# Performance work log

Measured on AMD Instinct MI355X. Metric: run time of the kernel, lower is better.

Reference implementation:

```python
import jax, jax.numpy as jnp
import numpy as np

B, L, DIM = 8, 512, 8          # batch, seq len, raw channels (value dim D = 2*DIM = 16)
ET, HID, H = 128, 128, 2       # embed_time, hidden_size, num_heads
MAXLEN = 512
NEG = -1e9


def setup_inputs() -> dict:
    key = jax.random.key(0)
    ks = jax.random.split(key, 40)
    def n(i, shape, s=0.05):
        return jax.random.normal(ks[i], shape, jnp.float32) * s
    vals = jax.random.normal(ks[0], (B, L, DIM), jnp.float32)
    msk = (jax.random.uniform(ks[1], (B, L, DIM)) > 0.2).astype(jnp.float32)
    x = jnp.concatenate([vals, msk], -1)                      # (B, L, 2*DIM)
    time_steps = jax.random.uniform(ks[2], (B, L), jnp.float32)
    return {
        'x': x, 'time_steps': time_steps,
        # learned time embedding: Linear(1, ET-1) periodic + Linear(1,1)
        'w_per': n(3, (1, ET - 1)), 'b_per': n(4, (ET - 1,)),
        'w_lin': n(5, (1, 1)), 'b_lin': n(6, (1,)),
        # MultiTimeAttention projections
        'Wq_t': n(7, (ET, ET)), 'bq_t': n(8, (ET,)),
        'Wk_t': n(9, (ET, ET)), 'bk_t': n(10, (ET,)),
        'Wo_t': n(11, (2 * DIM * H, HID)), 'bo_t': n(12, (HID,)),
        'pos_emb': n(13, (MAXLEN + 1, HID)), 'cls_emb': n(14, (1, HID)),
        # transformer block (BERT-style post-LN encoder layer, d_ff=HID)
        'tWq': n(15, (HID, HID)), 'tbq': n(16, (HID,)),
        'tWk': n(17, (HID, HID)), 'tbk': n(18, (HID,)),
        'tWv': n(19, (HID, HID)), 'tbv': n(20, (HID,)),
        'tWo': n(21, (HID, HID)), 'tbo': n(22, (HID,)),
        'ln1_g': jnp.ones((HID,), jnp.float32), 'ln1_b': jnp.zeros((HID,), jnp.float32),
        'fW1': n(23, (HID, HID)), 'fb1': n(24, (HID,)),
        'fW2': n(25, (HID, HID)), 'fb2': n(26, (HID,)),
        'ln2_g': jnp.ones((HID,), jnp.float32), 'ln2_b': jnp.zeros((HID,), jnp.float32),
        # BertPooler
        'pW': n(27, (HID, HID)), 'pb': n(28, (HID,)),
    }


def _time_emb(tt, w_per, b_per, w_lin, b_lin):
    tt = tt[..., None]                                        # (B, L, 1)
    return jnp.concatenate([tt @ w_lin + b_lin, jnp.sin(tt @ w_per + b_per)], -1)


def _ln(x, g, b, eps=1e-5):
    m = x.mean(-1, keepdims=True)
    v = ((x - m) ** 2).mean(-1, keepdims=True)
    return (x - m) / jnp.sqrt(v + eps) * g + b


def _mta(q_emb, k_emb, value, mask, Wq, bq, Wk, bk, Wo, bo):
    # MultiTimeAttention: scores broadcast to value-channel axis, softmax over keys
    D = value.shape[-1]
    dk = ET // H
    def split(e, W, b):
        p = e @ W + b
        return p.reshape(e.shape[0], -1, H, dk).transpose(0, 2, 1, 3)
    q = split(q_emb, Wq, bq)                                  # (Bq, H, Lq, dk)
    k = split(k_emb, Wk, bk)                                  # (B,  H, Lk, dk)
    scores = jnp.matmul(q, k.swapaxes(-1, -2)) / jnp.sqrt(jnp.float32(dk))  # (B,H,Lq,Lk)
    s5 = jnp.where(mask[:, None, None, :, :] == 0, NEG, scores[..., None])  # (B,H,Lq,Lk,D)
    p = jax.nn.softmax(s5, axis=-2)
    out = jnp.einsum('bhqkd,bkd->bhqd', p, value)             # (B, H, Lq, D)
    Bv = value.shape[0]
    out = out.transpose(0, 2, 1, 3).reshape(Bv, -1, H * D)
    return out @ Wo + bo


def _tblock(x, tWq, tbq, tWk, tbk, tWv, tbv, tWo, tbo, ln1_g, ln1_b,
            fW1, fb1, fW2, fb2, ln2_g, ln2_b):
    Bq, Lq, _ = x.shape
    dk = HID // H
    def heads(W, b):
        return (x @ W + b).reshape(Bq, Lq, H, dk).transpose(0, 2, 1, 3)
    q, k, v = heads(tWq, tbq), heads(tWk, tbk), heads(tWv, tbv)
    a = jax.nn.softmax(jnp.matmul(q, k.swapaxes(-1, -2)) / jnp.sqrt(jnp.float32(dk)), -1)
    o = jnp.matmul(a, v).transpose(0, 2, 1, 3).reshape(Bq, Lq, HID) @ tWo + tbo
    x = _ln(x + o, ln1_g, ln1_b)
    f = jax.nn.relu(x @ fW1 + fb1) @ fW2 + fb2
    return _ln(x + f, ln2_g, ln2_b)


def reference(x, time_steps, w_per, b_per, w_lin, b_lin,
              Wq_t, bq_t, Wk_t, bk_t, Wo_t, bo_t, pos_emb, cls_emb,
              tWq, tbq, tWk, tbk, tWv, tbv, tWo, tbo, ln1_g, ln1_b,
              fW1, fb1, fW2, fb2, ln2_g, ln2_b, pW, pb):
    Bx = x.shape[0]
    mask_half = x[:, :, DIM:]
    mask = jnp.concatenate([mask_half, mask_half], -1)        # (B, L, 2*DIM)
    key_e = _time_emb(time_steps, w_per, b_per, w_lin, b_lin)
    tq_e = _time_emb(time_steps, w_per, b_per, w_lin, b_lin)  # query_time_steps=None -> same
    cls_t = jnp.linspace(0.0, 1.0, 128, dtype=jnp.float32)[None]
    cls_q_e = _time_emb(cls_t, w_per, b_per, w_lin, b_lin)    # (1, 128, ET)
    cls_out = _mta(cls_q_e, key_e, x, mask, Wq_t, bq_t, Wk_t, bk_t, Wo_t, bo_t)
    out = _mta(tq_e, key_e, x, mask, Wq_t, bq_t, Wk_t, bk_t, Wo_t, bo_t)
    tb = (tWq, tbq, tWk, tbk, tWv, tbv, tWo, tbo, ln1_g, ln1_b,
          fW1, fb1, fW2, fb2, ln2_g, ln2_b)
    cls_repr = jnp.broadcast_to(cls_emb[None, :, :], (Bx, 1, HID))
    # encode(cls_out, is_pooling=True), pooling='bert': no pos emb, take token 0
    h = _tblock(jnp.concatenate([cls_repr, cls_out], 1), *tb)
    cls_pooling = jnp.tanh(h[:, 0] @ pW + pb)                 # (B, HID)
    # encode(out, is_pooling=False) [pretrain path]: pos emb + transformer, drop CLS
    h2 = jnp.concatenate([cls_repr, out], 1)                  # (B, L+1, HID)
    h2 = h2 + pos_emb[:h2.shape[1]][None]
    h2 = _tblock(h2, *tb)
    last_hidden_state = h2[:, 1:]                             # (B, L, HID)
    return cls_pooling, last_hidden_state
```

## Files before the change

### kernel.cpp

```cpp
#include <hip/hip_runtime.h>
#include <hip/hip_bf16.h>
#include <math.h>


static constexpr int NM_ = 8 * 513;
static constexpr int NC_ = 8 * 129;
static constexpr int NT_ = NM_ + NC_;

using bf = __hip_bfloat16;
typedef __attribute__((ext_vector_type(8))) short bf16x8;
typedef __attribute__((ext_vector_type(4))) short bf16x4;
typedef __attribute__((ext_vector_type(4))) float floatx4;
typedef __attribute__((ext_vector_type(8))) unsigned short ushortx8;

__device__ __forceinline__ float wave_reduce_sum(float v) {
    #pragma unroll
    for (int off = 32; off >= 1; off >>= 1) v += __shfl_xor(v, off);
    return v;
}
__device__ __forceinline__ float wave_reduce_max(float v) {
    #pragma unroll
    for (int off = 32; off >= 1; off >>= 1) v = fmaxf(v, __shfl_xor(v, off));
    return v;
}
__device__ __forceinline__ float u2f(unsigned short u) {
    return __uint_as_float(((unsigned)u) << 16);
}
__device__ __forceinline__ unsigned short f2u(float f) {
    unsigned u = __float_as_uint(f);
    return (unsigned short)((u + 0x7FFF + ((u >> 16) & 1)) >> 16);
}
__device__ __forceinline__ bf16x8 join8(bf16x4 lo, bf16x4 hi) {
    return __builtin_shufflevector(lo, hi, 0, 1, 2, 3, 4, 5, 6, 7);
}
__device__ __forceinline__ float rdin(const void* p, int i, int flag) {
    return flag ? u2f(((const unsigned short*)p)[i]) : ((const float*)p)[i];
}

struct PrepAll {
    const void* src[32]; int n[32]; int dstoff[32]; int conv[32];
    const void* wsrc[8]; unsigned short* wdst[8]; float wscale[8];
    const void* ts; const void* w_per; const void* b_per;
    const void* w_lin; const void* b_lin;
    unsigned short* key_e16;
    const unsigned short* det;
};
__global__ void prep_all_kernel(PrepAll a, float* dst) {
    int flag = (a.det[0] == 0x3F80u) ? 1 : 0;
    int blk = blockIdx.x, tid = threadIdx.x;
    if (blk < 8224) {
        int which = blk / 257, bi = blk - which * 257;
        if (!a.conv[which]) return;
        int i = bi * 256 + tid;
        if (i < a.n[which]) dst[a.dstoff[which] + i] = rdin(a.src[which], i, flag);
    } else if (blk < 8736) {
        int p = blk - 8224;
        int m = p >> 6;
        int idx = (p & 63) * 256 + tid;
        int c = idx >> 9;
        int l = (idx >> 3) & 63;
        int j = idx & 7;
        int k = (c >> 3) * 32 + (l >> 4) * 8 + j;
        int n = (c & 7) * 16 + (l & 15);
        a.wdst[m][idx] = f2u(rdin(a.wsrc[m], k * 128 + n, flag) * a.wscale[m]);
    } else {
        int p = blk - 8736;
        int row = p * 2 + (tid >> 7), j = tid & 127;
        float t = (row < 4096) ? rdin(a.ts, row, flag)
                               : (float)(row - 4096) * (1.0f / 127.0f);
        float v;
        if (j == 0) v = t * rdin(a.w_lin, 0, flag) + rdin(a.b_lin, 0, flag);
        else        v = sinf(t * rdin(a.w_per, j - 1, flag) + rdin(a.b_per, j - 1, flag));
        a.key_e16[row * 128 + j] = f2u(v);
    }
}

struct GemmM {
    const void* A[3]; const unsigned short* W[3]; const float* bias[3];
    unsigned short* C[3];
    int M[3]; int act[3]; int abf[3]; float bscale[3];
};
__global__ void __launch_bounds__(256)
gemm_mfma_kernel(GemmM p) {
    int y = blockIdx.y;
    const unsigned short* Wsw = p.W[y];
    const float* bias = p.bias[y];
    unsigned short* C = p.C[y];
    int M = p.M[y], act = p.act[y], abf = p.abf[y];
    float bscale = p.bscale[y];
    int m0 = blockIdx.x * 16;
    if (m0 >= M) return;
    __shared__ unsigned short As[16][136];
    int tid = threadIdx.x;
    if (abf) {
        const unsigned short* A = (const unsigned short*)p.A[y];
        int r = tid >> 4, c0 = (tid & 15) * 8;
        ushortx8 v = {0, 0, 0, 0, 0, 0, 0, 0};
        if (m0 + r < M) v = *(const ushortx8*)(A + (size_t)(m0 + r) * 128 + c0);
        *(ushortx8*)&As[r][c0] = v;
    } else {
        const float* A = (const float*)p.A[y];
        int r = tid >> 4, c0 = (tid & 15) * 8;
        float4 v0 = make_float4(0.f, 0.f, 0.f, 0.f), v1 = v0;
        if (m0 + r < M) {
            v0 = *(const float4*)(A + (size_t)(m0 + r) * 128 + c0);
            v1 = *(const float4*)(A + (size_t)(m0 + r) * 128 + c0 + 4);
        }
        *(ushort4*)&As[r][c0] = make_ushort4(f2u(v0.x), f2u(v0.y), f2u(v0.z), f2u(v0.w));
        *(ushort4*)&As[r][c0 + 4] = make_ushort4(f2u(v1.x), f2u(v1.y), f2u(v1.z), f2u(v1.w));
    }
    __syncthreads();

    int wv = tid >> 6, lane = tid & 63;
    floatx4 acc0 = {0.f, 0.f, 0.f, 0.f}, acc1 = acc0;
    int am = lane & 15, aq = lane >> 4;
    #pragma unroll
    for (int ks = 0; ks < 4; ++ks) {
        bf16x8 af = *(bf16x8*)&As[am][ks * 32 + aq * 8];
        const unsigned short* base = Wsw + ((size_t)ks * 8 + 2 * wv) * 512 + lane * 8;
        bf16x8 b0 = *(const bf16x8*)(base);
        bf16x8 b1 = *(const bf16x8*)(base + 512);
        acc0 = __builtin_amdgcn_mfma_f32_16x16x32_bf16(af, b0, acc0, 0, 0, 0);
        acc1 = __builtin_amdgcn_mfma_f32_16x16x32_bf16(af, b1, acc1, 0, 0, 0);
    }
    int col = lane & 15, rowb = (lane >> 4) * 4;
    #pragma unroll
    for (int t = 0; t < 2; ++t) {
        floatx4 acc = t ? acc1 : acc0;
        int n = wv * 32 + t * 16 + col;
        float bv = bias[n] * bscale;
        #pragma unroll
        for (int rg = 0; rg < 4; ++rg) {
            int m = m0 + rowb + rg;
            if (m < M) {
                float o = acc[rg] + bv;
                if (act) o = fmaxf(o, 0.f);
                C[(size_t)m * 128 + n] = f2u(o);
            }
        }
    }
}

__global__ void __launch_bounds__(256)
gemm_mfma_ln_kernel(const unsigned short* A, const unsigned short* Wsw, const float* bias,
                    const float* resid, const float* gam, const float* bet,
                    float* C) {
    int m0 = blockIdx.x * 16;
    __shared__ unsigned short As[16][136];
    __shared__ float redS[4][4][4], redQ[4][4][4];
    __shared__ float smean[16], sinv[16];
    int tid = threadIdx.x;
    {
        int r = tid >> 4, c0 = (tid & 15) * 8;
        ushortx8 v = *(const ushortx8*)(A + (size_t)(m0 + r) * 128 + c0);
        *(ushortx8*)&As[r][c0] = v;
    }
    __syncthreads();

    int wv = tid >> 6, lane = tid & 63;
    floatx4 acc0 = {0.f, 0.f, 0.f, 0.f}, acc1 = acc0;
    int am = lane & 15, aq = lane >> 4;
    #pragma unroll
    for (int ks = 0; ks < 4; ++ks) {
        bf16x8 af = *(bf16x8*)&As[am][ks * 32 + aq * 8];
        const unsigned short* base = Wsw + ((size_t)ks * 8 + 2 * wv) * 512 + lane * 8;
        bf16x8 b0 = *(const bf16x8*)(base);
        bf16x8 b1 = *(const bf16x8*)(base + 512);
        acc0 = __builtin_amdgcn_mfma_f32_16x16x32_bf16(af, b0, acc0, 0, 0, 0);
        acc1 = __builtin_amdgcn_mfma_f32_16x16x32_bf16(af, b1, acc1, 0, 0, 0);
    }

    int col = lane & 15, g = lane >> 4, rowb = g * 4;
    float ov[2][4];
    #pragma unroll
    for (int t = 0; t < 2; ++t) {
        int n = wv * 32 + t * 16 + col;
        float bv = bias[n];
        floatx4 acc = t ? acc1 : acc0;
        #pragma unroll
        for (int rg = 0; rg < 4; ++rg)
            ov[t][rg] = acc[rg] + bv + resid[(size_t)(m0 + rowb + rg) * 128 + n];
    }
    #pragma unroll
    for (int rg = 0; rg < 4; ++rg) {
        float s = ov[0][rg] + ov[1][rg];
        float q = ov[0][rg] * ov[0][rg] + ov[1][rg] * ov[1][rg];
        #pragma unroll
        for (int off = 8; off >= 1; off >>= 1) {
            s += __shfl_xor(s, off);
            q += __shfl_xor(q, off);
        }
        if ((lane & 15) == 0) { redS[wv][g][rg] = s; redQ[wv][g][rg] = q; }
    }
    __syncthreads();
    if (tid < 16) {
        int gg = tid >> 2, rg = tid & 3;
        float s = redS[0][gg][rg] + redS[1][gg][rg] + redS[2][gg][rg] + redS[3][gg][rg];
        float q = redQ[0][gg][rg] + redQ[1][gg][rg] + redQ[2][gg][rg] + redQ[3][gg][rg];
        float mean = s * 0.0078125f;
        float var = q * 0.0078125f - mean * mean;
        smean[tid] = mean;
        sinv[tid] = rsqrtf(var + 1e-5f);
    }
    __syncthreads();
    #pragma unroll
    for (int t = 0; t < 2; ++t) {
        int n = wv * 32 + t * 16 + col;
        float gm = gam[n], bb = bet[n];
        #pragma unroll
        for (int rg = 0; rg < 4; ++rg) {
            int row = rowb + rg;
            C[(size_t)(m0 + row) * 128 + n] = (ov[t][rg] - smean[row]) * sinv[row] * gm + bb;
        }
    }
}

__global__ void __launch_bounds__(256)
ffn_ln_kernel(const float* x1, const unsigned short* W1, const float* b1,
              const unsigned short* W2, const float* b2,
              const float* gam, const float* bet, float* dout, float* x2c) {
    int m0 = blockIdx.x * 16;
    __shared__ float Xs[16][128];
    __shared__ unsigned short As[16][136];
    __shared__ unsigned short Hs[16][136];
    __shared__ float redS[4][4][4], redQ[4][4][4];
    __shared__ float smean[16], sinv[16];
    int tid = threadIdx.x;
    {
        int r = tid >> 4, c0 = (tid & 15) * 8;
        float4 v0 = *(const float4*)(x1 + (size_t)(m0 + r) * 128 + c0);
        float4 v1 = *(const float4*)(x1 + (size_t)(m0 + r) * 128 + c0 + 4);
        *(float4*)&Xs[r][c0] = v0;
        *(float4*)&Xs[r][c0 + 4] = v1;
        *(ushort4*)&As[r][c0] = make_ushort4(f2u(v0.x), f2u(v0.y), f2u(v0.z), f2u(v0.w));
        *(ushort4*)&As[r][c0 + 4] = make_ushort4(f2u(v1.x), f2u(v1.y), f2u(v1.z), f2u(v1.w));
    }
    __syncthreads();

    int wv = tid >> 6, lane = tid & 63;
    int am = lane & 15, aq = lane >> 4;
    int col = lane & 15, g = lane >> 4, rowb = g * 4;

    {
        floatx4 acc0 = {0.f, 0.f, 0.f, 0.f}, acc1 = acc0;
        #pragma unroll
        for (int ks = 0; ks < 4; ++ks) {
            bf16x8 af = *(bf16x8*)&As[am][ks * 32 + aq * 8];
            const unsigned short* base = W1 + ((size_t)ks * 8 + 2 * wv) * 512 + lane * 8;
            bf16x8 bb0 = *(const bf16x8*)(base);
            bf16x8 bb1 = *(const bf16x8*)(base + 512);
            acc0 = __builtin_amdgcn_mfma_f32_16x16x32_bf16(af, bb0, acc0, 0, 0, 0);
            acc1 = __builtin_amdgcn_mfma_f32_16x16x32_bf16(af, bb1, acc1, 0, 0, 0);
        }
        #pragma unroll
        for (int t = 0; t < 2; ++t) {
            int n = wv * 32 + t * 16 + col;
            float bv = b1[n];
            floatx4 acc = t ? acc1 : acc0;
            #pragma unroll
            for (int rg = 0; rg < 4; ++rg)
                Hs[rowb + rg][n] = f2u(fmaxf(acc[rg] + bv, 0.f));
        }
    }
    __syncthreads();

    floatx4 acc0 = {0.f, 0.f, 0.f, 0.f}, acc1 = acc0;
    #pragma unroll
    for (int ks = 0; ks < 4; ++ks) {
        bf16x8 af = *(bf16x8*)&Hs[am][ks * 32 + aq * 8];
        const unsigned short* base = W2 + ((size_t)ks * 8 + 2 * wv) * 512 + lane * 8;
        bf16x8 bb0 = *(const bf16x8*)(base);
        bf16x8 bb1 = *(const bf16x8*)(base + 512);
        acc0 = __builtin_amdgcn_mfma_f32_16x16x32_bf16(af, bb0, acc0, 0, 0, 0);
        acc1 = __builtin_amdgcn_mfma_f32_16x16x32_bf16(af, bb1, acc1, 0, 0, 0);
    }
    float ov[2][4];
    #pragma unroll
    for (int t = 0; t < 2; ++t) {
        int n = wv * 32 + t * 16 + col;
        float bv = b2[n];
        floatx4 acc = t ? acc1 : acc0;
        #pragma unroll
        for (int rg = 0; rg < 4; ++rg)
            ov[t][rg] = acc[rg] + bv + Xs[rowb + rg][n];
    }
    #pragma unroll
    for (int rg = 0; rg < 4; ++rg) {
        float s = ov[0][rg] + ov[1][rg];
        float q = ov[0][rg] * ov[0][rg] + ov[1][rg] * ov[1][rg];
        #pragma unroll
        for (int off = 8; off >= 1; off >>= 1) {
            s += __shfl_xor(s, off);
            q += __shfl_xor(q, off);
        }
        if ((lane & 15) == 0) { redS[wv][g][rg] = s; redQ[wv][g][rg] = q; }
    }
    __syncthreads();
    if (tid < 16) {
        int gg = tid >> 2, rg = tid & 3;
        float s = redS[0][gg][rg] + redS[1][gg][rg] + redS[2][gg][rg] + redS[3][gg][rg];
        float q = redQ[0][gg][rg] + redQ[1][gg][rg] + redQ[2][gg][rg] + redQ[3][gg][rg];
        float mean = s * 0.0078125f;
        float var = q * 0.0078125f - mean * mean;
        smean[tid] = mean;
        sinv[tid] = rsqrtf(var + 1e-5f);
    }
    __syncthreads();
    #pragma unroll
    for (int t = 0; t < 2; ++t) {
        int n = wv * 32 + t * 16 + col;
        float gm = gam[n], bb = bet[n];
        #pragma unroll
        for (int rg = 0; rg < 4; ++rg) {
            int row = rowb + rg;
            int m = m0 + row;
            float val = (ov[t][rg] - smean[row]) * sinv[row] * gm + bb;
            if (m < NM_) {
                int b = m / 513, r = m - b * 513;
                if (r >= 1)
                    dout[1024 + (size_t)b * 65536 + (size_t)(r - 1) * 128 + n] = val;
            } else {
                int mc = m - NM_;
                int b = mc / 129, r = mc - b * 129;
                if (r == 0) x2c[b * 128 + n] = val;
            }
        }
    }
}

__global__ void mta_out_assemble_kernel(const float* att, const float* W, const float* bias,
                                        const float* cls_emb, const float* pos, float* xin) {
    int tid = threadIdx.x;
    if (blockIdx.x == 320) {
        for (int e = tid; e < 16 * 128; e += 256) {
            int i = e >> 7, j = e & 127;
            int b = i >> 1;
            if ((i & 1) == 0) xin[(size_t)(b * 513) * 128 + j] = cls_emb[j] + pos[j];
            else              xin[(size_t)(4104 + b * 129) * 128 + j] = cls_emb[j];
        }
        return;
    }
    int m0 = blockIdx.x * 16;
    __shared__ float As[16][36];
    int r = tid >> 4, gq = tid & 15, c0 = gq * 8;
    if (gq < 2) {
        const float* src = att + (size_t)(m0 + r) * 32 + gq * 16;
        *(float4*)&As[r][gq * 16]      = *(const float4*)(src);
        *(float4*)&As[r][gq * 16 + 4]  = *(const float4*)(src + 4);
        *(float4*)&As[r][gq * 16 + 8]  = *(const float4*)(src + 8);
        *(float4*)&As[r][gq * 16 + 12] = *(const float4*)(src + 12);
    }
    __syncthreads();
    float acc[8];
    #pragma unroll
    for (int j = 0; j < 8; ++j) acc[j] = bias[c0 + j];
    #pragma unroll 8
    for (int k = 0; k < 32; ++k) {
        float a = As[r][k];
        const float4 w0 = *(const float4*)(W + (size_t)k * 128 + c0);
        const float4 w1 = *(const float4*)(W + (size_t)k * 128 + c0 + 4);
        acc[0] = fmaf(a, w0.x, acc[0]); acc[1] = fmaf(a, w0.y, acc[1]);
        acc[2] = fmaf(a, w0.z, acc[2]); acc[3] = fmaf(a, w0.w, acc[3]);
        acc[4] = fmaf(a, w1.x, acc[4]); acc[5] = fmaf(a, w1.y, acc[5]);
        acc[6] = fmaf(a, w1.z, acc[6]); acc[7] = fmaf(a, w1.w, acc[7]);
    }
    int m = m0 + r;
    size_t dstrow;
    if (m < 1024) {
        int b = m >> 7, rr = m & 127;
        dstrow = (size_t)(4104 + b * 129 + 1 + rr);
    } else {
        int mm = m - 1024;
        int b = mm >> 9, rr = mm & 511;
        dstrow = (size_t)(b * 513 + 1 + rr);
        const float* pr = pos + (size_t)(1 + rr) * 128 + c0;
        float4 p0 = *(const float4*)(pr);
        float4 p1 = *(const float4*)(pr + 4);
        acc[0] += p0.x; acc[1] += p0.y; acc[2] += p0.z; acc[3] += p0.w;
        acc[4] += p1.x; acc[5] += p1.y; acc[6] += p1.z; acc[7] += p1.w;
    }
    *(float4*)(xin + dstrow * 128 + c0) = make_float4(acc[0], acc[1], acc[2], acc[3]);
    *(float4*)(xin + dstrow * 128 + c0 + 4) = make_float4(acc[4], acc[5], acc[6], acc[7]);
}

__global__ void __launch_bounds__(256)
mta_att_kernel(const unsigned short* qp_cls, const unsigned short* qp_main,
               const unsigned short* kp, const float* x,
               float* att_cls, float* att_mn) {
    int is_cls = (blockIdx.x >= 32);
    int qt = is_cls ? (blockIdx.x - 32) : blockIdx.x;
    int h = blockIdx.y, b = blockIdx.z;
    int tid = threadIdx.x, lane = tid & 63, wv = tid >> 6;
    __shared__ unsigned short Qs[16][72];
    __shared__ unsigned short KV[64][72];
    __shared__ unsigned short sp[16][520];
    __shared__ unsigned short Bt[16][520];
    float* xv = (float*)&KV[0][0];
    int q0 = qt * 16;

    if (tid < 128) {
        int r = tid >> 3, c0 = (tid & 7) * 8;
        const unsigned short* qrow = is_cls ? (qp_cls + (size_t)(q0 + r) * 128 + h * 64)
                                            : (qp_main + (size_t)(b * 512 + q0 + r) * 128 + h * 64);
        *(ushortx8*)&Qs[r][c0] = *(const ushortx8*)(qrow + c0);
    }
    __syncthreads();

    bf16x8 qf0, qf1;
    {
        int m = lane & 15, g = lane >> 4;
        qf0 = *(const bf16x8*)&Qs[m][g * 8];
        qf1 = *(const bf16x8*)&Qs[m][32 + g * 8];
    }

    for (int kt = 0; kt < 8; ++kt) {
        int k0 = kt * 64;
        {
            int kk = tid >> 3, e0 = (tid & 7) * 8;
            #pragma unroll
            for (int it = 0; it < 2; ++it, kk += 32)
                *(ushortx8*)&KV[kk][e0] =
                    *(const ushortx8*)(kp + (size_t)(b * 512 + k0 + kk) * 128 + h * 64 + e0);
        }
        __syncthreads();
        int kn = lane & 15, g = lane >> 4;
        floatx4 acc = {0.f, 0.f, 0.f, 0.f};
        {
            bf16x8 b0 = *(const bf16x8*)&KV[wv * 16 + kn][g * 8];
            acc = __builtin_amdgcn_mfma_f32_16x16x32_bf16(qf0, b0, acc, 0, 0, 0);
            bf16x8 b1 = *(const bf16x8*)&KV[wv * 16 + kn][32 + g * 8];
            acc = __builtin_amdgcn_mfma_f32_16x16x32_bf16(qf1, b1, acc, 0, 0, 0);
        }
        int colk = k0 + wv * 16 + kn;
        #pragma unroll
        for (int rg = 0; rg < 4; ++rg) sp[g * 4 + rg][colk] = f2u(acc[rg]);
        __syncthreads();
    }

    for (int rr = wv; rr < 16; rr += 4) {
        float m = -1e30f;
        for (int k = lane; k < 512; k += 64) m = fmaxf(m, u2f(sp[rr][k]));
        m = wave_reduce_max(m);
        for (int k = lane; k < 512; k += 64) sp[rr][k] = f2u(expf(u2f(sp[rr][k]) - m));
    }

    for (int kt = 0; kt < 8; ++kt) {
        int k0 = kt * 64;
        __syncthreads();
        {
            int kk = tid >> 2, c0 = (tid & 3) * 4;
            float4 v = *(const float4*)(x + (size_t)(b * 512 + k0 + kk) * 16 + c0);
            xv[kk * 17 + c0] = v.x; xv[kk * 17 + c0 + 1] = v.y;
            xv[kk * 17 + c0 + 2] = v.z; xv[kk * 17 + c0 + 3] = v.w;
        }
        __syncthreads();
        {
            int c = tid & 15, k4 = (tid >> 4) * 4;
            #pragma unroll
            for (int i = 0; i < 4; ++i) {
                int k = k4 + i;
                float val = (c < 8) ? xv[k * 17 + c] * xv[k * 17 + 8 + c]
                                    : xv[k * 17 + c];
                Bt[c][k0 + k] = f2u(val);
            }
        }
    }
    __syncthreads();

    floatx4 macc = {0.f, 0.f, 0.f, 0.f};
    {
        int mq = lane & 15, g = lane >> 4;
        #pragma unroll
        for (int cc = 0; cc < 4; ++cc) {
            int koff = (wv + cc * 4) * 32;
            bf16x8 af = *(const bf16x8*)&sp[mq][koff + g * 8];
            bf16x8 bfv = *(const bf16x8*)&Bt[mq][koff + g * 8];
            macc = __builtin_amdgcn_mfma_f32_16x16x32_bf16(af, bfv, macc, 0, 0, 0);
        }
    }
    float* redC = (float*)&KV[0][0];
    float* Cfull = redC + 1024;
    #pragma unroll
    for (int rg = 0; rg < 4; ++rg) redC[(wv * 64 + lane) * 4 + rg] = macc[rg];
    __syncthreads();
    {
        int l = tid >> 2, rg = tid & 3;
        float s = redC[l * 4 + rg] + redC[(64 + l) * 4 + rg]
                + redC[(128 + l) * 4 + rg] + redC[(192 + l) * 4 + rg];
        int row = (l >> 4) * 4 + rg, c = l & 15;
        Cfull[row * 16 + c] = s;
    }
    __syncthreads();
    if (tid < 128) {
        int r = tid >> 3, c = tid & 7;
        float num = Cfull[r * 16 + c];
        float den = Cfull[r * 16 + 8 + c];
        int row = q0 + r;
        float* dst = is_cls ? (att_cls + (size_t)(b * 128 + row) * 32)
                            : (att_mn + (size_t)(b * 512 + row) * 32);
        dst[h * 16 + c] = num / den;
        dst[h * 16 + 8 + c] = 1.0f;
    }
}

__global__ void __launch_bounds__(256)
tb_att_kernel(const unsigned short* qp, const unsigned short* kp,
              const unsigned short* vp, unsigned short* outp) {
    int is_cls = (blockIdx.x >= 33);
    int qt = is_cls ? blockIdx.x - 33 : blockIdx.x;
    int h = blockIdx.y, b = blockIdx.z;
    int Lq = is_cls ? 129 : 513;
    int base = is_cls ? (4104 + b * 129) : (b * 513);
    int nkt = is_cls ? 3 : 9;
    int tid = threadIdx.x, lane = tid & 63, wv = tid >> 6;
    __shared__ unsigned short Qs[16][72];
    __shared__ unsigned short KV[64][72];
    __shared__ unsigned short sp[16][588];
    __shared__ float rinv[16];
    int q0 = qt * 16;

    if (tid < 128) {
        int r = tid >> 3, c0 = (tid & 7) * 8;
        int qr = q0 + r;
        ushortx8 v = {0, 0, 0, 0, 0, 0, 0, 0};
        if (qr < Lq) v = *(const ushortx8*)(qp + (size_t)(base + qr) * 128 + h * 64 + c0);
        *(ushortx8*)&Qs[r][c0] = v;
    }
    __syncthreads();

    bf16x8 qf0, qf1;
    {
        int m = lane & 15, g = lane >> 4;
        qf0 = *(const bf16x8*)&Qs[m][g * 8];
        qf1 = *(const bf16x8*)&Qs[m][32 + g * 8];
    }

    for (int kt = 0; kt < nkt; ++kt) {
        int k0 = kt * 64;
        {
            int kk = tid >> 3, e0 = (tid & 7) * 8;
            #pragma unroll
            for (int it = 0; it < 2; ++it, kk += 32) {
                int krow = k0 + kk;
                ushortx8 v = {0, 0, 0, 0, 0, 0, 0, 0};
                if (krow < Lq) v = *(const ushortx8*)(kp + (size_t)(base + krow) * 128 + h * 64 + e0);
                *(ushortx8*)&KV[kk][e0] = v;
            }
        }
        __syncthreads();
        int kn = lane & 15, g = lane >> 4;
        floatx4 acc = {0.f, 0.f, 0.f, 0.f};
        {
            bf16x8 b0 = *(const bf16x8*)&KV[wv * 16 + kn][g * 8];
            acc = __builtin_amdgcn_mfma_f32_16x16x32_bf16(qf0, b0, acc, 0, 0, 0);
            bf16x8 b1 = *(const bf16x8*)&KV[wv * 16 + kn][32 + g * 8];
            acc = __builtin_amdgcn_mfma_f32_16x16x32_bf16(qf1, b1, acc, 0, 0, 0);
        }
        int colk = k0 + wv * 16 + kn;
        #pragma unroll
        for (int rg = 0; rg < 4; ++rg)
            sp[g * 4 + rg][colk] = f2u((colk < Lq) ? acc[rg] : -1e30f);
        __syncthreads();
    }

    int kend = nkt * 64;
    for (int rr = wv; rr < 16; rr += 4) {
        float m = -1e30f;
        for (int k = lane; k < kend; k += 64) m = fmaxf(m, u2f(sp[rr][k]));
        m = wave_reduce_max(m);
        float sum = 0.f;
        for (int k = lane; k < kend; k += 64) {
            float e = expf(u2f(sp[rr][k]) - m);
            sp[rr][k] = f2u(e);
            sum += e;
        }
        sum = wave_reduce_sum(sum);
        if (lane == 0) rinv[rr] = 1.f / sum;
    }

    floatx4 oacc = {0.f, 0.f, 0.f, 0.f};
    for (int kt = 0; kt < nkt; ++kt) {
        int k0 = kt * 64;
        __syncthreads();
        {
            int kk = tid & 31, e0 = (tid >> 5) * 8;
            #pragma unroll
            for (int it = 0; it < 2; ++it, kk += 32) {
                int krow = k0 + kk;
                ushortx8 v = {0, 0, 0, 0, 0, 0, 0, 0};
                if (krow < Lq) v = *(const ushortx8*)(vp + (size_t)(base + krow) * 128 + h * 64 + e0);
                #pragma unroll
                for (int j = 0; j < 8; ++j) KV[e0 + j][kk] = v[j];
            }
        }
        __syncthreads();
        int dn = lane & 15, g = lane >> 4;
        #pragma unroll
        for (int c = 0; c < 2; ++c) {
            bf16x4 plo = *(const bf16x4*)&sp[lane & 15][k0 + c * 32 + g * 8];
            bf16x4 phi = *(const bf16x4*)&sp[lane & 15][k0 + c * 32 + g * 8 + 4];
            bf16x8 vf = *(const bf16x8*)&KV[wv * 16 + dn][c * 32 + g * 8];
            oacc = __builtin_amdgcn_mfma_f32_16x16x32_bf16(join8(plo, phi), vf, oacc, 0, 0, 0);
        }
    }
    int dcol = wv * 16 + (lane & 15), g = lane >> 4;
    #pragma unroll
    for (int rg = 0; rg < 4; ++rg) {
        int q = g * 4 + rg;
        int qr = q0 + q;
        if (qr < Lq)
            outp[(size_t)(base + qr) * 128 + h * 64 + dcol] = f2u(oacc[rg] * rinv[q]);
    }
}

__global__ void pool_tanh_kernel(const float* x2c, const float* W, const float* bias,
                                 float* dout) {
    __shared__ float As[8][132];
    int tid = threadIdx.x;
    int r = tid >> 5, g = tid & 31;
    for (int c = g; c < 128; c += 32) As[r][c] = x2c[(size_t)r * 128 + c];
    __syncthreads();
    int rr = tid >> 5, c0 = (tid & 31) * 4;
    float acc[4];
    #pragma unroll
    for (int j = 0; j < 4; ++j) acc[j] = bias[c0 + j];
    for (int k = 0; k < 128; ++k) {
        float a = As[rr][k];
        const float4 w0 = *(const float4*)(W + (size_t)k * 128 + c0);
        acc[0] = fmaf(a, w0.x, acc[0]); acc[1] = fmaf(a, w0.y, acc[1]);
        acc[2] = fmaf(a, w0.z, acc[2]); acc[3] = fmaf(a, w0.w, acc[3]);
    }
    *(float4*)(dout + (size_t)rr * 128 + c0) =
        make_float4(tanhf(acc[0]), tanhf(acc[1]), tanhf(acc[2]), tanhf(acc[3]));
}

extern "C" void kernel_launch(void* const* d_in, const int* in_sizes, int n_in,
                              void* d_out, int out_size, void* d_ws, size_t ws_size,
                              hipStream_t stream) {
    float* w = (float*)d_ws;
    size_t off = 0;
    auto alloc = [&](size_t n) {
        float* p = w + off;
        off += (n + 3) & ~(size_t)3;
        return p;
    };
    auto allocU = [&](size_t n) { return (unsigned short*)alloc((n + 1) / 2); };

    PrepAll pa{};
    int nn = n_in < 32 ? n_in : 32;
    float* fin[32];
    const int needconv[32] = {1,0,0,0,0,0, 0,1, 0,1, 1,1, 1,1, 0,1, 0,1, 0,1,
                              0,1, 1,1, 0,1, 0,1, 1,1, 1,1};
    for (int i = 0; i < nn; ++i) {
        pa.src[i] = d_in[i];
        pa.n[i] = in_sizes[i];
        fin[i] = alloc(in_sizes[i]);
        pa.dstoff[i] = (int)(fin[i] - w);
        pa.conv[i] = needconv[i];
    }
    for (int i = nn; i < 32; ++i) { pa.src[i] = nullptr; pa.n[i] = 0; pa.dstoff[i] = 0; pa.conv[i] = 0; }

    const float* x       = fin[0];
    const float* bq_t    = fin[7];
    const float* bk_t    = fin[9];
    const float* Wo_t    = fin[10]; const float* bo_t = fin[11];
    const float* pos_emb = fin[12]; const float* cls_emb = fin[13];
    const float* tbq = fin[15]; const float* tbk = fin[17]; const float* tbv = fin[19];
    const float* tbo = fin[21];
    const float* ln1_g = fin[22]; const float* ln1_b = fin[23];
    const float* fb1 = fin[25]; const float* fb2 = fin[27];
    const float* ln2_g = fin[28]; const float* ln2_b = fin[29];
    const float* pW = fin[30]; const float* pb = fin[31];

    const int widx[8] = {8, 6, 14, 16, 18, 20, 24, 26};
    unsigned short* wsw[8];
    for (int i = 0; i < 8; ++i) {
        wsw[i] = allocU(16384);
        pa.wsrc[i] = d_in[widx[i]];
        pa.wdst[i] = wsw[i];
        pa.wscale[i] = (i == 1 || i == 2) ? 0.125f : 1.0f;
    }
    pa.ts = d_in[1]; pa.w_per = d_in[2]; pa.b_per = d_in[3];
    pa.w_lin = d_in[4]; pa.b_lin = d_in[5];
    pa.det = (const unsigned short*)d_in[22];

    unsigned short* key_e16 = allocU(4224 * 128);
    unsigned short* cls_e16 = key_e16 + 4096 * 128;
    pa.key_e16 = key_e16;

    unsigned short* qp_main16 = allocU(4096 * 128);
    unsigned short* kp_main16 = allocU(4096 * 128);
    unsigned short* qp_cls16  = allocU(128 * 128);
    float* att_all = alloc(5120 * 32);
    float* att_cls = att_all;
    float* att_mn  = att_all + 1024 * 32;
    float* xin     = alloc((size_t)NT_ * 128);
    unsigned short* tbq16 = allocU((size_t)NT_ * 128);
    unsigned short* tbk16 = allocU((size_t)NT_ * 128);
    unsigned short* tbv16 = allocU((size_t)NT_ * 128);
    unsigned short* tba16 = allocU((size_t)NT_ * 128);
    float* tb_x1   = alloc((size_t)NT_ * 128);
    float* x2c     = alloc(8 * 128);
    (void)ws_size;

    float* outf = (float*)d_out;

    prep_all_kernel<<<10848, 256, 0, stream>>>(pa, w);

    {
        GemmM p{};
        p.A[0] = key_e16; p.W[0] = wsw[0]; p.bias[0] = bk_t; p.C[0] = kp_main16;
        p.M[0] = 4096; p.act[0] = 0; p.abf[0] = 1; p.bscale[0] = 1.f;
        p.A[1] = key_e16; p.W[1] = wsw[1]; p.bias[1] = bq_t; p.C[1] = qp_main16;
        p.M[1] = 4096; p.act[1] = 0; p.abf[1] = 1; p.bscale[1] = 0.125f;
        p.A[2] = cls_e16; p.W[2] = wsw[1]; p.bias[2] = bq_t; p.C[2] = qp_cls16;
        p.M[2] = 128; p.act[2] = 0; p.abf[2] = 1; p.bscale[2] = 0.125f;
        gemm_mfma_kernel<<<dim3(256, 3), 256, 0, stream>>>(p);
    }

    mta_att_kernel<<<dim3(40, 2, 8), 256, 0, stream>>>(qp_cls16, qp_main16, kp_main16,
                                                       x, att_cls, att_mn);

    mta_out_assemble_kernel<<<321, 256, 0, stream>>>(att_all, Wo_t, bo_t, cls_emb, pos_emb, xin);

    {
        GemmM p{};
        const unsigned short* Ws[3] = {wsw[2], wsw[3], wsw[4]};
        const float* bs[3] = {tbq, tbk, tbv};
        unsigned short* Cs[3] = {tbq16, tbk16, tbv16};
        float sc[3] = {0.125f, 1.f, 1.f};
        for (int y = 0; y < 3; ++y) {
            p.A[y] = xin; p.W[y] = Ws[y]; p.bias[y] = bs[y]; p.C[y] = Cs[y];
            p.M[y] = NT_; p.act[y] = 0; p.abf[y] = 0; p.bscale[y] = sc[y];
        }
        gemm_mfma_kernel<<<dim3((NT_ + 15) / 16, 3), 256, 0, stream>>>(p);
    }

    tb_att_kernel<<<dim3(42, 2, 8), 256, 0, stream>>>(tbq16, tbk16, tbv16, tba16);

    gemm_mfma_ln_kernel<<<NT_ / 16, 256, 0, stream>>>(tba16, wsw[5], tbo, xin, ln1_g, ln1_b, tb_x1);

    ffn_ln_kernel<<<NT_ / 16, 256, 0, stream>>>(tb_x1, wsw[6], fb1, wsw[7], fb2,
                                                ln2_g, ln2_b, outf, x2c);

    pool_tanh_kernel<<<1, 256, 0, stream>>>(x2c, pW, pb, outf);
}
```

Baseline: 197.3 us.

## Fuse MTA output projection with QKV GEMMs and attn-out with FFN and pooler

Merges the MTA output/assemble step into the transformer Q/K/V projection kernel, so the bf16 input tile is built in shared memory and the three GEMMs run in one block. The attention-output+LN1 kernel is merged with the FFN+LN2 kernel, and the pooler tanh is folded in for CLS rows. This cuts the kernel launch count from 8 to 5 and removes the fp32 xin re-read and the tb_x1 round trip through global memory. The cost is fewer, heavier blocks (321 of them), so each block does serial work. The pooler now runs a 128-length serial dot product per thread inside a single block per batch.

Measured after the change: 189.1 us. 4.1% less time.

```diff
diff --git a/kernel.cpp b/kernel.cpp
--- a/kernel.cpp
+++ b/kernel.cpp
@@ -78,7 +78,7 @@
 struct GemmM {
     const void* A[3]; const unsigned short* W[3]; const float* bias[3];
     unsigned short* C[3];
-    int M[3]; int act[3]; int abf[3]; float bscale[3];
+    int M[3]; float bscale[3];
 };
 __global__ void __launch_bounds__(256)
 gemm_mfma_kernel(GemmM p) {
@@ -86,28 +86,18 @@
     const unsigned short* Wsw = p.W[y];
     const float* bias = p.bias[y];
     unsigned short* C = p.C[y];
-    int M = p.M[y], act = p.act[y], abf = p.abf[y];
+    int M = p.M[y];
     float bscale = p.bscale[y];
     int m0 = blockIdx.x * 16;
     if (m0 >= M) return;
     __shared__ unsigned short As[16][136];
     int tid = threadIdx.x;
-    if (abf) {
+    {
         const unsigned short* A = (const unsigned short*)p.A[y];
         int r = tid >> 4, c0 = (tid & 15) * 8;
         ushortx8 v = {0, 0, 0, 0, 0, 0, 0, 0};
         if (m0 + r < M) v = *(const ushortx8*)(A + (size_t)(m0 + r) * 128 + c0);
         *(ushortx8*)&As[r][c0] = v;
-    } else {
-        const float* A = (const float*)p.A[y];
-        int r = tid >> 4, c0 = (tid & 15) * 8;
-        float4 v0 = make_float4(0.f, 0.f, 0.f, 0.f), v1 = v0;
-        if (m0 + r < M) {
-            v0 = *(const float4*)(A + (size_t)(m0 + r) * 128 + c0);
-            v1 = *(const float4*)(A + (size_t)(m0 + r) * 128 + c0 + 4);
-        }
-        *(ushort4*)&As[r][c0] = make_ushort4(f2u(v0.x), f2u(v0.y), f2u(v0.z), f2u(v0.w));
-        *(ushort4*)&As[r][c0 + 4] = make_ushort4(f2u(v1.x), f2u(v1.y), f2u(v1.z), f2u(v1.w));
     }
     __syncthreads();
 
@@ -132,54 +122,154 @@
         #pragma unroll
         for (int rg = 0; rg < 4; ++rg) {
             int m = m0 + rowb + rg;
-            if (m < M) {
-                float o = acc[rg] + bv;
-                if (act) o = fmaxf(o, 0.f);
-                C[(size_t)m * 128 + n] = f2u(o);
-            }
+            if (m < M) C[(size_t)m * 128 + n] = f2u(acc[rg] + bv);
         }
     }
 }
 
 __global__ void __launch_bounds__(256)
-gemm_mfma_ln_kernel(const unsigned short* A, const unsigned short* Wsw, const float* bias,
-                    const float* resid, const float* gam, const float* bet,
-                    float* C) {
+mta_qkv_kernel(const float* att, const float* Wo, const float* bo,
+               const float* cls_emb, const float* pos, float* xin,
+               const unsigned short* Wq, const unsigned short* Wk, const unsigned short* Wv,
+               const float* bq, const float* bk, const float* bv_,
+               unsigned short* outq, unsigned short* outk, unsigned short* outv) {
+    int m0 = blockIdx.x * 16;
+    __shared__ float As32[16][36];
+    __shared__ unsigned short As[16][136];
+    int tid = threadIdx.x;
+    int r = tid >> 4, g = tid & 15, c0 = g * 8;
+
+    int R = m0 + r;
+    int srow, prow;
+    if (R < NM_) {
+        int b = R / 513, rr = R - b * 513;
+        srow = (rr == 0) ? -1 : 1024 + b * 512 + (rr - 1);
+        prow = rr;
+    } else {
+        int mc = R - NM_;
+        int b = mc / 129, rr = mc - b * 129;
+        srow = (rr == 0) ? -1 : b * 128 + (rr - 1);
+        prow = -1;
+    }
+    if (g < 2 && srow >= 0) {
+        const float* src = att + (size_t)srow * 32 + g * 16;
+        *(float4*)&As32[r][g * 16]      = *(const float4*)(src);
+        *(float4*)&As32[r][g * 16 + 4]  = *(const float4*)(src + 4);
+        *(float4*)&As32[r][g * 16 + 8]  = *(const float4*)(src + 8);
+        *(float4*)&As32[r][g * 16 + 12] = *(const float4*)(src + 12);
+    }
+    __syncthreads();
+
+    float acc[8];
+    if (srow < 0) {
+        #pragma unroll
+        for (int j = 0; j < 8; ++j) acc[j] = cls_emb[c0 + j];
+    } else {
+        #pragma unroll
+        for (int j = 0; j < 8; ++j) acc[j] = bo[c0 + j];
+        #pragma unroll 8
+        for (int k = 0; k < 32; ++k) {
+            float a = As32[r][k];
+            const float4 w0 = *(const float4*)(Wo + (size_t)k * 128 + c0);
+            const float4 w1 = *(const float4*)(Wo + (size_t)k * 128 + c0 + 4);
+            acc[0] = fmaf(a, w0.x, acc[0]); acc[1] = fmaf(a, w0.y, acc[1]);
+            acc[2] = fmaf(a, w0.z, acc[2]); acc[3] = fmaf(a, w0.w, acc[3]);
+            acc[4] = fmaf(a, w1.x, acc[4]); acc[5] = fmaf(a, w1.y, acc[5]);
+            acc[6] = fmaf(a, w1.z, acc[6]); acc[7] = fmaf(a, w1.w, acc[7]);
+        }
+    }
+    if (prow >= 0) {
+        const float* pr = pos + (size_t)prow * 128 + c0;
+        float4 p0 = *(const float4*)(pr);
+        float4 p1 = *(const float4*)(pr + 4);
+        acc[0] += p0.x; acc[1] += p0.y; acc[2] += p0.z; acc[3] += p0.w;
+        acc[4] += p1.x; acc[5] += p1.y; acc[6] += p1.z; acc[7] += p1.w;
+    }
+    *(float4*)(xin + (size_t)R * 128 + c0) = make_float4(acc[0], acc[1], acc[2], acc[3]);
+    *(float4*)(xin + (size_t)R * 128 + c0 + 4) = make_float4(acc[4], acc[5], acc[6], acc[7]);
+    *(ushort4*)&As[r][c0] = make_ushort4(f2u(acc[0]), f2u(acc[1]), f2u(acc[2]), f2u(acc[3]));
+    *(ushort4*)&As[r][c0 + 4] = make_ushort4(f2u(acc[4]), f2u(acc[5]), f2u(acc[6]), f2u(acc[7]));
+    __syncthreads();
+
+    int wv = tid >> 6, lane = tid & 63;
+    int am = lane & 15, aq = lane >> 4;
+    int col = lane & 15, rowb = (lane >> 4) * 4;
+    const unsigned short* Ws[3] = {Wq, Wk, Wv};
+    const float* bs[3] = {bq, bk, bv_};
+    float bsc[3] = {0.125f, 1.f, 1.f};
+    unsigned short* Cs[3] = {outq, outk, outv};
+    #pragma unroll
+    for (int y = 0; y < 3; ++y) {
+        floatx4 acc0 = {0.f, 0.f, 0.f, 0.f}, acc1 = acc0;
+        #pragma unroll
+        for (int ks = 0; ks < 4; ++ks) {
+            bf16x8 af = *(bf16x8*)&As[am][ks * 32 + aq * 8];
+            const unsigned short* base = Ws[y] + ((size_t)ks * 8 + 2 * wv) * 512 + lane * 8;
+            bf16x8 b0 = *(const bf16x8*)(base);
+            bf16x8 b1 = *(const bf16x8*)(base + 512);
+            acc0 = __builtin_amdgcn_mfma_f32_16x16x32_bf16(af, b0, acc0, 0, 0, 0);
+            acc1 = __builtin_amdgcn_mfma_f32_16x16x32_bf16(af, b1, acc1, 0, 0, 0);
+        }
+        #pragma unroll
+        for (int t = 0; t < 2; ++t) {
+            floatx4 a2 = t ? acc1 : acc0;
+            int n = wv * 32 + t * 16 + col;
+            float bvv = bs[y][n] * bsc[y];
+            #pragma unroll
+            for (int rg = 0; rg < 4; ++rg)
+                Cs[y][(size_t)(m0 + rowb + rg) * 128 + n] = f2u(a2[rg] + bvv);
+        }
+    }
+}
+
+__global__ void __launch_bounds__(256)
+attnout_ffn_kernel(const unsigned short* A, const unsigned short* Wao, const float* bao,
+                   const float* resid, const float* g1, const float* b1ln,
+                   const unsigned short* W1, const float* fb1,
+                   const unsigned short* W2, const float* fb2,
+                   const float* g2, const float* b2ln,
+                   const float* pW, const float* pb, float* dout) {
     int m0 = blockIdx.x * 16;
     __shared__ unsigned short As[16][136];
+    __shared__ float Xs[16][128];
+    __shared__ unsigned short Hs[16][136];
     __shared__ float redS[4][4][4], redQ[4][4][4];
     __shared__ float smean[16], sinv[16];
+    __shared__ float x2row[128];
+    __shared__ int poolb;
     int tid = threadIdx.x;
+    if (tid == 0) poolb = -1;
     {
         int r = tid >> 4, c0 = (tid & 15) * 8;
-        ushortx8 v = *(const ushortx8*)(A + (size_t)(m0 + r) * 128 + c0);
-        *(ushortx8*)&As[r][c0] = v;
+        *(ushortx8*)&As[r][c0] = *(const ushortx8*)(A + (size_t)(m0 + r) * 128 + c0);
     }
     __syncthreads();
 
     int wv = tid >> 6, lane = tid & 63;
-    floatx4 acc0 = {0.f, 0.f, 0.f, 0.f}, acc1 = acc0;
     int am = lane & 15, aq = lane >> 4;
-    #pragma unroll
-    for (int ks = 0; ks < 4; ++ks) {
-        bf16x8 af = *(bf16x8*)&As[am][ks * 32 + aq * 8];
-        const unsigned short* base = Wsw + ((size_t)ks * 8 + 2 * wv) * 512 + lane * 8;
-        bf16x8 b0 = *(const bf16x8*)(base);
-        bf16x8 b1 = *(const bf16x8*)(base + 512);
-        acc0 = __builtin_amdgcn_mfma_f32_16x16x32_bf16(af, b0, acc0, 0, 0, 0);
-        acc1 = __builtin_amdgcn_mfma_f32_16x16x32_bf16(af, b1, acc1, 0, 0, 0);
-    }
-
     int col = lane & 15, g = lane >> 4, rowb = g * 4;
+
     float ov[2][4];
-    #pragma unroll
-    for (int t = 0; t < 2; ++t) {
-        int n = wv * 32 + t * 16 + col;
-        float bv = bias[n];
-        floatx4 acc = t ? acc1 : acc0;
-        #pragma unroll
-        for (int rg = 0; rg < 4; ++rg)
-            ov[t][rg] = acc[rg] + bv + resid[(size_t)(m0 + rowb + rg) * 128 + n];
+    {
+        floatx4 acc0 = {0.f, 0.f, 0.f, 0.f}, acc1 = acc0;
+        #pragma unroll
+        for (int ks = 0; ks < 4; ++ks) {
+            bf16x8 af = *(bf16x8*)&As[am][ks * 32 + aq * 8];
+            const unsigned short* base = Wao + ((size_t)ks * 8 + 2 * wv) * 512 + lane * 8;
+            bf16x8 bb0 = *(const bf16x8*)(base);
+            bf16x8 bb1 = *(const bf16x8*)(base + 512);
+            acc0 = __builtin_amdgcn_mfma_f32_16x16x32_bf16(af, bb0, acc0, 0, 0, 0);
+            acc1 = __builtin_amdgcn_mfma_f32_16x16x32_bf16(af, bb1, acc1, 0, 0, 0);
+        }
+        #pragma unroll
+        for (int t = 0; t < 2; ++t) {
+            int n = wv * 32 + t * 16 + col;
+            float bv = bao[n];
+            floatx4 acc = t ? acc1 : acc0;
+            #pragma unroll
+            for (int rg = 0; rg < 4; ++rg)
+                ov[t][rg] = acc[rg] + bv + resid[(size_t)(m0 + rowb + rg) * 128 + n];
+        }
     }
     #pragma unroll
     for (int rg = 0; rg < 4; ++rg) {
@@ -206,40 +296,16 @@
     #pragma unroll
     for (int t = 0; t < 2; ++t) {
         int n = wv * 32 + t * 16 + col;
-        float gm = gam[n], bb = bet[n];
+        float gm = g1[n], bb = b1ln[n];
         #pragma unroll
         for (int rg = 0; rg < 4; ++rg) {
             int row = rowb + rg;
-            C[(size_t)(m0 + row) * 128 + n] = (ov[t][rg] - smean[row]) * sinv[row] * gm + bb;
-        }
-    }
-}
-
-__global__ void __launch_bounds__(256)
-ffn_ln_kernel(const float* x1, const unsigned short* W1, const float* b1,
-              const unsigned short* W2, const float* b2,
-              const float* gam, const float* bet, float* dout, float* x2c) {
-    int m0 = blockIdx.x * 16;
-    __shared__ float Xs[16][128];
-    __shared__ unsigned short As[16][136];
-    __shared__ unsigned short Hs[16][136];
-    __shared__ float redS[4][4][4], redQ[4][4][4];
-    __shared__ float smean[16], sinv[16];
-    int tid = threadIdx.x;
-    {
-        int r = tid >> 4, c0 = (tid & 15) * 8;
-        float4 v0 = *(const float4*)(x1 + (size_t)(m0 + r) * 128 + c0);
-        float4 v1 = *(const float4*)(x1 + (size_t)(m0 + r) * 128 + c0 + 4);
-        *(float4*)&Xs[r][c0] = v0;
-        *(float4*)&Xs[r][c0 + 4] = v1;
-        *(ushort4*)&As[r][c0] = make_ushort4(f2u(v0.x), f2u(v0.y), f2u(v0.z), f2u(v0.w));
-        *(ushort4*)&As[r][c0 + 4] = make_ushort4(f2u(v1.x), f2u(v1.y), f2u(v1.z), f2u(v1.w));
-    }
-    __syncthreads();
-
-    int wv = tid >> 6, lane = tid & 63;
-    int am = lane & 15, aq = lane >> 4;
-    int col = lane & 15, g = lane >> 4, rowb = g * 4;
+            float val = (ov[t][rg] - smean[row]) * sinv[row] * gm + bb;
+            Xs[row][n] = val;
+            As[row][n] = f2u(val);
+        }
+    }
+    __syncthreads();
 
     {
         floatx4 acc0 = {0.f, 0.f, 0.f, 0.f}, acc1 = acc0;
@@ -255,7 +321,7 @@
         #pragma unroll
         for (int t = 0; t < 2; ++t) {
             int n = wv * 32 + t * 16 + col;
-            float bv = b1[n];
+            float bv = fb1[n];
             floatx4 acc = t ? acc1 : acc0;
             #pragma unroll
             for (int rg = 0; rg < 4; ++rg)
@@ -274,11 +340,10 @@
         acc0 = __builtin_amdgcn_mfma_f32_16x16x32_bf16(af, bb0, acc0, 0, 0, 0);
         acc1 = __builtin_amdgcn_mfma_f32_16x16x32_bf16(af, bb1, acc1, 0, 0, 0);
     }
-    float ov[2][4];
     #pragma unroll
     for (int t = 0; t < 2; ++t) {
         int n = wv * 32 + t * 16 + col;
-        float bv = b2[n];
+        float bv = fb2[n];
         floatx4 acc = t ? acc1 : acc0;
         #pragma unroll
         for (int rg = 0; rg < 4; ++rg)
@@ -309,7 +374,7 @@
     #pragma unroll
     for (int t = 0; t < 2; ++t) {
         int n = wv * 32 + t * 16 + col;
-        float gm = gam[n], bb = bet[n];
+        float gm = g2[n], bb = b2ln[n];
         #pragma unroll
         for (int rg = 0; rg < 4; ++rg) {
             int row = rowb + rg;
@@ -322,65 +387,19 @@
             } else {
                 int mc = m - NM_;
                 int b = mc / 129, r = mc - b * 129;
-                if (r == 0) x2c[b * 128 + n] = val;
+                if (r == 0) {
+                    x2row[n] = val;
+                    if (n == 0) poolb = b;
+                }
             }
         }
     }
-}
-
-__global__ void mta_out_assemble_kernel(const float* att, const float* W, const float* bias,
-                                        const float* cls_emb, const float* pos, float* xin) {
-    int tid = threadIdx.x;
-    if (blockIdx.x == 320) {
-        for (int e = tid; e < 16 * 128; e += 256) {
-            int i = e >> 7, j = e & 127;
-            int b = i >> 1;
-            if ((i & 1) == 0) xin[(size_t)(b * 513) * 128 + j] = cls_emb[j] + pos[j];
-            else              xin[(size_t)(4104 + b * 129) * 128 + j] = cls_emb[j];
-        }
-        return;
-    }
-    int m0 = blockIdx.x * 16;
-    __shared__ float As[16][36];
-    int r = tid >> 4, gq = tid & 15, c0 = gq * 8;
-    if (gq < 2) {
-        const float* src = att + (size_t)(m0 + r) * 32 + gq * 16;
-        *(float4*)&As[r][gq * 16]      = *(const float4*)(src);
-        *(float4*)&As[r][gq * 16 + 4]  = *(const float4*)(src + 4);
-        *(float4*)&As[r][gq * 16 + 8]  = *(const float4*)(src + 8);
-        *(float4*)&As[r][gq * 16 + 12] = *(const float4*)(src + 12);
-    }
-    __syncthreads();
-    float acc[8];
-    #pragma unroll
-    for (int j = 0; j < 8; ++j) acc[j] = bias[c0 + j];
-    #pragma unroll 8
-    for (int k = 0; k < 32; ++k) {
-        float a = As[r][k];
-        const float4 w0 = *(const float4*)(W + (size_t)k * 128 + c0);
-        const float4 w1 = *(const float4*)(W + (size_t)k * 128 + c0 + 4);
-        acc[0] = fmaf(a, w0.x, acc[0]); acc[1] = fmaf(a, w0.y, acc[1]);
-        acc[2] = fmaf(a, w0.z, acc[2]); acc[3] = fmaf(a, w0.w, acc[3]);
-        acc[4] = fmaf(a, w1.x, acc[4]); acc[5] = fmaf(a, w1.y, acc[5]);
-        acc[6] = fmaf(a, w1.z, acc[6]); acc[7] = fmaf(a, w1.w, acc[7]);
-    }
-    int m = m0 + r;
-    size_t dstrow;
-    if (m < 1024) {
-        int b = m >> 7, rr = m & 127;
-        dstrow = (size_t)(4104 + b * 129 + 1 + rr);
-    } else {
-        int mm = m - 1024;
-        int b = mm >> 9, rr = mm & 511;
-        dstrow = (size_t)(b * 513 + 1 + rr);
-        const float* pr = pos + (size_t)(1 + rr) * 128 + c0;
-        float4 p0 = *(const float4*)(pr);
-        float4 p1 = *(const float4*)(pr + 4);
-        acc[0] += p0.x; acc[1] += p0.y; acc[2] += p0.z; acc[3] += p0.w;
-        acc[4] += p1.x; acc[5] += p1.y; acc[6] += p1.z; acc[7] += p1.w;
-    }
-    *(float4*)(xin + dstrow * 128 + c0) = make_float4(acc[0], acc[1], acc[2], acc[3]);
-    *(float4*)(xin + dstrow * 128 + c0 + 4) = make_float4(acc[4], acc[5], acc[6], acc[7]);
+    __syncthreads();
+    if (poolb >= 0 && tid < 128) {
+        float acc = pb[tid];
+        for (int k = 0; k < 128; ++k) acc = fmaf(x2row[k], pW[(size_t)k * 128 + tid], acc);
+        dout[(size_t)poolb * 128 + tid] = tanhf(acc);
+    }
 }
 
 __global__ void __launch_bounds__(256)
@@ -613,27 +632,6 @@
     }
 }
 
-__global__ void pool_tanh_kernel(const float* x2c, const float* W, const float* bias,
-                                 float* dout) {
-    __shared__ float As[8][132];
-    int tid = threadIdx.x;
-    int r = tid >> 5, g = tid & 31;
-    for (int c = g; c < 128; c += 32) As[r][c] = x2c[(size_t)r * 128 + c];
-    __syncthreads();
-    int rr = tid >> 5, c0 = (tid & 31) * 4;
-    float acc[4];
-    #pragma unroll
-    for (int j = 0; j < 4; ++j) acc[j] = bias[c0 + j];
-    for (int k = 0; k < 128; ++k) {
-        float a = As[rr][k];
-        const float4 w0 = *(const float4*)(W + (size_t)k * 128 + c0);
-        acc[0] = fmaf(a, w0.x, acc[0]); acc[1] = fmaf(a, w0.y, acc[1]);
-        acc[2] = fmaf(a, w0.z, acc[2]); acc[3] = fmaf(a, w0.w, acc[3]);
-    }
-    *(float4*)(dout + (size_t)rr * 128 + c0) =
-        make_float4(tanhf(acc[0]), tanhf(acc[1]), tanhf(acc[2]), tanhf(acc[3]));
-}
-
 extern "C" void kernel_launch(void* const* d_in, const int* in_sizes, int n_in,
                               void* d_out, int out_size, void* d_ws, size_t ws_size,
                               hipStream_t stream) {
@@ -699,8 +697,6 @@
     unsigned short* tbk16 = allocU((size_t)NT_ * 128);
     unsigned short* tbv16 = allocU((size_t)NT_ * 128);
     unsigned short* tba16 = allocU((size_t)NT_ * 128);
-    float* tb_x1   = alloc((size_t)NT_ * 128);
-    float* x2c     = alloc(8 * 128);
     (void)ws_size;
 
     float* outf = (float*)d_out;
@@ -710,38 +706,24 @@
     {
         GemmM p{};
         p.A[0] = key_e16; p.W[0] = wsw[0]; p.bias[0] = bk_t; p.C[0] = kp_main16;
-        p.M[0] = 4096; p.act[0] = 0; p.abf[0] = 1; p.bscale[0] = 1.f;
+        p.M[0] = 4096; p.bscale[0] = 1.f;
         p.A[1] = key_e16; p.W[1] = wsw[1]; p.bias[1] = bq_t; p.C[1] = qp_main16;
-        p.M[1] = 4096; p.act[1] = 0; p.abf[1] = 1; p.bscale[1] = 0.125f;
+        p.M[1] = 4096; p.bscale[1] = 0.125f;
         p.A[2] = cls_e16; p.W[2] = wsw[1]; p.bias[2] = bq_t; p.C[2] = qp_cls16;
-        p.M[2] = 128; p.act[2] = 0; p.abf[2] = 1; p.bscale[2] = 0.125f;
+        p.M[2] = 128; p.bscale[2] = 0.125f;
         gemm_mfma_kernel<<<dim3(256, 3), 256, 0, stream>>>(p);
     }
 
     mta_att_kernel<<<dim3(40, 2, 8), 256, 0, stream>>>(qp_cls16, qp_main16, kp_main16,
                                                        x, att_cls, att_mn);
 
-    mta_out_assemble_kernel<<<321, 256, 0, stream>>>(att_all, Wo_t, bo_t, cls_emb, pos_emb, xin);
-
-    {
-        GemmM p{};
-        const unsigned short* Ws[3] = {wsw[2], wsw[3], wsw[4]};
-        const float* bs[3] = {tbq, tbk, tbv};
-        unsigned short* Cs[3] = {tbq16, tbk16, tbv16};
-        float sc[3] = {0.125f, 1.f, 1.f};
-        for (int y = 0; y < 3; ++y) {
-            p.A[y] = xin; p.W[y] = Ws[y]; p.bias[y] = bs[y]; p.C[y] = Cs[y];
-            p.M[y] = NT_; p.act[y] = 0; p.abf[y] = 0; p.bscale[y] = sc[y];
-        }
-        gemm_mfma_kernel<<<dim3((NT_ + 15) / 16, 3), 256, 0, stream>>>(p);
-    }
+    mta_qkv_kernel<<<321, 256, 0, stream>>>(att_all, Wo_t, bo_t, cls_emb, pos_emb, xin,
+                                            wsw[2], wsw[3], wsw[4], tbq, tbk, tbv,
+                                            tbq16, tbk16, tbv16);
 
     tb_att_kernel<<<dim3(42, 2, 8), 256, 0, stream>>>(tbq16, tbk16, tbv16, tba16);
 
-    gemm_mfma_ln_kernel<<<NT_ / 16, 256, 0, stream>>>(tba16, wsw[5], tbo, xin, ln1_g, ln1_b, tb_x1);
-
-    ffn_ln_kernel<<<NT_ / 16, 256, 0, stream>>>(tb_x1, wsw[6], fb1, wsw[7], fb2,
-                                                ln2_g, ln2_b, outf, x2c);
-
-    pool_tanh_kernel<<<1, 256, 0, stream>>>(x2c, pW, pb, outf);
-}
+    attnout_ffn_kernel<<<321, 256, 0, stream>>>(tba16, wsw[5], tbo, xin, ln1_g, ln1_b,
+                                                wsw[6], fb1, wsw[7], fb2, ln2_g, ln2_b,
+                                                pW, pb, outf);
+}
```
